# Kernel tuning notes

Measured on AMD Instinct MI355X. Metric: run time of the kernel, lower is better.

Reference implementation:

```python
import jax, jax.numpy as jnp
import numpy as np

EPS = 1e-5
NUM_CLASSES = 35
STYLE_LEN = 128


def conv3x3(x, w, b):
    # x: [B,C,H,W], w: [O,I,3,3] (OIHW), SAME padding, stride 1
    y = jax.lax.conv_general_dilated(x, w, (1, 1), 'SAME',
                                     dimension_numbers=('NCHW', 'OIHW', 'NCHW'))
    return y + b[None, :, None, None]


def instance_norm(x):
    # InstanceNorm2d(affine=False): per-sample, per-channel over H,W; biased var
    mu = jnp.mean(x, axis=(2, 3), keepdims=True)
    var = jnp.mean((x - mu) ** 2, axis=(2, 3), keepdims=True)
    return (x - mu) * jax.lax.rsqrt(var + EPS)


def setup_inputs() -> dict:
    key = jax.random.key(0)
    ks = jax.random.split(key, 20)
    B, C, H, W = 4, 256, 128, 256
    J, S = NUM_CLASSES, STYLE_LEN
    s = 0.05
    inp = {
        'x': jax.random.normal(ks[0], (B, C, H, W), jnp.float32),
        'seg_labels': jax.random.randint(ks[1], (B, H, W), 0, J),
        'style_codes': jax.random.normal(ks[2], (B, J, S), jnp.float32),
        # per-class FC: fc_w[j] is [out,in] like torch Linear
        'fc_w': jax.random.normal(ks[3], (J, S, S), jnp.float32) * s,
        'fc_b': jax.random.normal(ks[4], (J, S), jnp.float32) * s,
        'conv_gamma_w': jax.random.normal(ks[5], (C, S, 3, 3), jnp.float32) * s,
        'conv_gamma_b': jax.random.normal(ks[6], (C,), jnp.float32) * s,
        'conv_beta_w': jax.random.normal(ks[7], (C, S, 3, 3), jnp.float32) * s,
        'conv_beta_b': jax.random.normal(ks[8], (C,), jnp.float32) * s,
        # SPADE (sean=True): mlp_shared conv label_nc->128, then gamma/beta 128->C
        'mlp_w': jax.random.normal(ks[9], (128, J, 3, 3), jnp.float32) * s,
        'mlp_b': jax.random.normal(ks[10], (128,), jnp.float32) * s,
        'sp_gamma_w': jax.random.normal(ks[11], (C, 128, 3, 3), jnp.float32) * s,
        'sp_gamma_b': jax.random.normal(ks[12], (C,), jnp.float32) * s,
        'sp_beta_w': jax.random.normal(ks[13], (C, 128, 3, 3), jnp.float32) * s,
        'sp_beta_b': jax.random.normal(ks[14], (C,), jnp.float32) * s,
        'blending_gamma': jnp.zeros((1,), jnp.float32),
        'blending_beta': jnp.zeros((1,), jnp.float32),
    }
    return inp


def reference(x, seg_labels, style_codes, fc_w, fc_b,
              conv_gamma_w, conv_gamma_b, conv_beta_w, conv_beta_b,
              mlp_w, mlp_b, sp_gamma_w, sp_gamma_b, sp_beta_w, sp_beta_b,
              blending_gamma, blending_beta):
    # one-hot segmap [B,J,H,W]; same resolution as x so nearest interp is identity
    segmap = jax.nn.one_hot(seg_labels, NUM_CLASSES, axis=1, dtype=x.dtype)

    normalized = instance_norm(x)

    # per-class style FC: mu[b,j,:] = relu(fc_w[j] @ style_codes[b,j] + fc_b[j])
    mu = jax.nn.relu(jnp.einsum('bjd,jod->bjo', style_codes, fc_w) + fc_b[None])
    # gather-compute-scatter: each pixel receives the style vector of its class
    middle_avg = jnp.einsum('bjhw,bjc->bchw', segmap, mu)  # [B,128,H,W]

    gamma_avg = conv3x3(middle_avg, conv_gamma_w, conv_gamma_b)
    beta_avg = conv3x3(middle_avg, conv_beta_w, conv_beta_b)

    # SPADE branch (sean): gamma/beta from segmap
    actv = jax.nn.relu(conv3x3(segmap, mlp_w, mlp_b))
    gamma_spade = conv3x3(actv, sp_gamma_w, sp_gamma_b)
    beta_spade = conv3x3(actv, sp_beta_w, sp_beta_b)

    ga = jax.nn.sigmoid(blending_gamma)[0]
    ba = jax.nn.sigmoid(blending_beta)[0]
    gamma_final = ga * gamma_avg + (1 - ga) * gamma_spade
    beta_final = ba * beta_avg + (1 - ba) * beta_spade
    return normalized * (1 + gamma_final) + beta_final
```

## Files before the change

kernel.cpp:

```cpp
#include <hip/hip_runtime.h>
#include <stdint.h>

typedef __attribute__((ext_vector_type(8))) short short8;
typedef __attribute__((ext_vector_type(4))) float f32x4;

#define HP 130
#define WPAD 258
#define CIN 256

#define AS1 __attribute__((address_space(1)))
#define AS3 __attribute__((address_space(3)))

__device__ __forceinline__ unsigned short f2bf(float f) {
  unsigned int x = __float_as_uint(f);
  x = x + 0x7fffu + ((x >> 16) & 1u);
  return (unsigned short)(x >> 16);
}

__global__ __launch_bounds__(128) void k_mu(const float* __restrict__ sty,
    const float* __restrict__ fcw, const float* __restrict__ fcb,
    float* __restrict__ mu)
{
  int bj = blockIdx.x;
  int b = bj / 35, j = bj - 35 * b;
  int o = threadIdx.x;
  __shared__ float ss[128];
  ss[o] = sty[((size_t)b * 35 + j) * 128 + o];
  __syncthreads();
  const float4* wr = (const float4*)(fcw + ((size_t)j * 128 + o) * 128);
  const float4* sv = (const float4*)ss;
  float acc = fcb[j * 128 + o];
  #pragma unroll 8
  for (int d = 0; d < 32; ++d) {
    float4 wv = wr[d], s4 = sv[d];
    acc += wv.x * s4.x + wv.y * s4.y + wv.z * s4.z + wv.w * s4.w;
  }
  mu[((size_t)b * 35 + j) * 128 + o] = fmaxf(acc, 0.f);
}

__global__ __launch_bounds__(256) void k_prep(const float* __restrict__ mlpw,
    float* __restrict__ mlpT,
    const float* __restrict__ cgb, const float* __restrict__ cbb,
    const float* __restrict__ sgb, const float* __restrict__ sbb,
    const float* __restrict__ blg, const float* __restrict__ blb,
    float* __restrict__ bias)
{
  int t = blockIdx.x * 256 + threadIdx.x;
  if (t < 40320) {
    int o = t & 127;
    int jt = t >> 7;
    mlpT[(size_t)jt * 128 + o] = mlpw[((size_t)o * 35 + (jt / 9)) * 9 + (jt % 9)];
  }
  if (t < 256) {
    float ga = 1.f / (1.f + expf(-blg[0]));
    float ba = 1.f / (1.f + expf(-blb[0]));
    bias[t]       = ga * cgb[t] + (1.f - ga) * sgb[t];
    bias[256 + t] = ba * cbb[t] + (1.f - ba) * sbb[t];
  }
}

__global__ __launch_bounds__(256) void k_pack(
    const float* __restrict__ cgw, const float* __restrict__ cbw,
    const float* __restrict__ sgw, const float* __restrict__ sbw,
    const float* __restrict__ blg, const float* __restrict__ blb,
    unsigned short* __restrict__ Wp)
{
  int gid = blockIdx.x * 256 + threadIdx.x;
  int lane = gid & 63;
  int cc = (gid >> 6) & 7;
  int rest = gid >> 9;
  int tap = rest % 9;
  int vf = rest / 9;
  int v = vf * 16 + (lane & 15);
  int c = v >> 1, g = v & 1;
  int ci0 = cc * 32 + (lane >> 4) * 8;
  float ga = 1.f / (1.f + expf(-blg[0]));
  float ba = 1.f / (1.f + expf(-blb[0]));
  float sc = g ? ba : ga;
  const float* wavg = g ? cbw : cgw;
  const float* wsp  = g ? sbw : sgw;
  union { uint4 v4; unsigned short s[8]; } u;
  #pragma unroll
  for (int jj = 0; jj < 8; ++jj) {
    int ci = ci0 + jj;
    float val;
    if (ci < 128) val = sc * wavg[((size_t)c * 128 + ci) * 9 + tap];
    else          val = (1.f - sc) * wsp[((size_t)c * 128 + (ci - 128)) * 9 + tap];
    u.s[jj] = f2bf(val);
  }
  int vfgrp = vf >> 2, mfi = vf & 3;
  uint4* dst = (uint4*)Wp + ((size_t)(((vfgrp * 8 + cc) * 9 + tap) * 4 + mfi)) * 64 + lane;
  *dst = u.v4;
}

__global__ __launch_bounds__(256) void k_stats(const float* __restrict__ x,
                                               float* __restrict__ stats)
{
  int bc = blockIdx.x;
  const float* p = x + (size_t)bc * 32768;
  int t = threadIdx.x;
  float s = 0.f, s2 = 0.f;
  #pragma unroll 4
  for (int i = 0; i < 32; ++i) {
    float4 v = *(const float4*)(p + (size_t)i * 1024 + t * 4);
    s  += v.x + v.y + v.z + v.w;
    s2 += v.x * v.x + v.y * v.y + v.z * v.z + v.w * v.w;
  }
  #pragma unroll
  for (int off2 = 32; off2 > 0; off2 >>= 1) {
    s  += __shfl_down(s, off2);
    s2 += __shfl_down(s2, off2);
  }
  __shared__ float red[8];
  int lane = t & 63, wv = t >> 6;
  if (lane == 0) { red[wv] = s; red[4 + wv] = s2; }
  __syncthreads();
  if (t == 0) {
    float S  = red[0] + red[1] + red[2] + red[3];
    float S2 = red[4] + red[5] + red[6] + red[7];
    float mean = S * (1.f / 32768.f);
    float var  = S2 * (1.f / 32768.f) - mean * mean;
    stats[bc] = mean;
    stats[1024 + bc] = rsqrtf(var + 1e-5f);
  }
}

__global__ __launch_bounds__(256) void k_halo(uint4* __restrict__ U4)
{
  int t = blockIdx.x * 256 + threadIdx.x;
  if (t >= 98816) return;
  int sub = t & 31, pi = t >> 5;
  int b = pi / 772, r = pi - b * 772;
  int h, w;
  if (r < 258)      { h = 0;   w = r; }
  else if (r < 516) { h = 129; w = r - 258; }
  else if (r < 644) { h = r - 516 + 1; w = 0; }
  else              { h = r - 644 + 1; w = 257; }
  U4[((size_t)(b * HP + h) * WPAD + w) * 32 + sub] = (uint4){0, 0, 0, 0};
}

__global__ __launch_bounds__(256) void k_build(const int* __restrict__ seg,
    const float* __restrict__ mu, const float* __restrict__ mlpT,
    const float* __restrict__ mlpb, unsigned short* __restrict__ U)
{
  int blk = blockIdx.x;
  int b = blk >> 12, rem = blk & 4095;
  int h = rem >> 5, w0 = (rem & 31) << 3;
  int t = threadIdx.x;
  int p = t >> 5, q = t & 31;
  int w = w0 + p;
  unsigned short* up = U + (((size_t)(b * HP + h + 1)) * WPAD + (w + 1)) * CIN;
  union { uint4 v4; unsigned short s[8]; } u;
  if (q < 16) {
    int lab = seg[((size_t)b * 128 + h) * 256 + w];
    const float4* mrow = (const float4*)(mu + ((size_t)(b * 35 + lab)) * 128 + q * 8);
    float4 v0 = mrow[0], v1 = mrow[1];
    u.s[0] = f2bf(v0.x); u.s[1] = f2bf(v0.y); u.s[2] = f2bf(v0.z); u.s[3] = f2bf(v0.w);
    u.s[4] = f2bf(v1.x); u.s[5] = f2bf(v1.y); u.s[6] = f2bf(v1.z); u.s[7] = f2bf(v1.w);
    *(uint4*)(up + q * 8) = u.v4;
  } else {
    int o0 = (q - 16) * 8;
    float a[8];
    #pragma unroll
    for (int j = 0; j < 8; ++j) a[j] = mlpb[o0 + j];
    #pragma unroll
    for (int kh = 0; kh < 3; ++kh) {
      int hh = h + kh - 1;
      if ((unsigned)hh < 128u) {
        #pragma unroll
        for (int kw = 0; kw < 3; ++kw) {
          int ww = w + kw - 1;
          if ((unsigned)ww < 256u) {
            int lab2 = seg[((size_t)b * 128 + hh) * 256 + ww];
            const float4* wr = (const float4*)(mlpT + ((size_t)lab2 * 9 + kh * 3 + kw) * 128 + o0);
            float4 v0 = wr[0], v1 = wr[1];
            a[0] += v0.x; a[1] += v0.y; a[2] += v0.z; a[3] += v0.w;
            a[4] += v1.x; a[5] += v1.y; a[6] += v1.z; a[7] += v1.w;
          }
        }
      }
    }
    #pragma unroll
    for (int j = 0; j < 8; ++j) u.s[j] = f2bf(fmaxf(a[j], 0.f));
    *(uint4*)(up + 128 + o0) = u.v4;
  }
}


#define WAITV_(vm, lg) asm volatile("s_waitcnt vmcnt(" #vm ") lgkmcnt(" #lg ")" ::: "memory")
#define WAITV(vm, lg) do { WAITV_(vm, lg); __builtin_amdgcn_sched_barrier(0); } while (0)
#define WAITL(lg) do { asm volatile("s_waitcnt lgkmcnt(" #lg ")" ::: "memory"); __builtin_amdgcn_sched_barrier(0); } while (0)

#define MM(AS, BS, H) do {                                                     \
    __builtin_amdgcn_s_setprio(1);                                             \
    _Pragma("unroll")                                                          \
    for (int mf_ = 0; mf_ < 4; ++mf_)                                          \
      _Pragma("unroll")                                                        \
      for (int nf_ = 0; nf_ < 4; ++nf_)                                        \
        acc[mf_][(H) * 4 + nf_] = __builtin_amdgcn_mfma_f32_16x16x32_bf16(     \
            afr##AS[mf_], bfr##BS[nf_], acc[mf_][(H) * 4 + nf_], 0, 0, 0);     \
    __builtin_amdgcn_s_setprio(0);                                             \
  } while (0)

#define LOADA(NS) do {                                                         \
    aptr += 4096;                                                              \
    afr##NS[0] = *(const short8*)(aptr);                                       \
    afr##NS[1] = *(const short8*)(aptr + 1024);                                \
    afr##NS[2] = *(const short8*)(aptr + 2048);                                \
    afr##NS[3] = *(const short8*)(aptr + 3072);                                \
  } while (0)

#define LOADB(NS, T, H) do {                                                   \
    bfr##NS[0] = *(const short8*)(lbuf + off[T] + (H) * 4096);                 \
    bfr##NS[1] = *(const short8*)(lbuf + off[T] + (H) * 4096 + 1024);          \
    bfr##NS[2] = *(const short8*)(lbuf + off[T] + (H) * 4096 + 2048);          \
    bfr##NS[3] = *(const short8*)(lbuf + off[T] + (H) * 4096 + 3072);          \
  } while (0)

#define STG(SI) do {                                                           \
    __builtin_amdgcn_global_load_lds((const AS1 unsigned int*)gsrc[SI],        \
        (AS3 unsigned int*)((SI) < 6 ? (stbw + (SI) * 4096) : (stb + 24576)),  \
        16, 0, 0);                                                             \
    gsrc[SI] += 64;                                                            \
  } while (0)

__global__ __launch_bounds__(256, 2) void k_conv(
    const float* __restrict__ x, const uint4* __restrict__ U,
    const char* __restrict__ Wp, const float* __restrict__ bias,
    const float* __restrict__ stats, float* __restrict__ out)
{
  int bid = blockIdx.x;
  int xcd = bid & 7, i0 = bid >> 3;
  int pt = xcd * 128 + (i0 >> 1);
  int mt = i0 & 1;
  int b = pt >> 8, rem = pt & 255;
  int h0 = rem >> 1, w0 = (rem & 1) << 7;
  int tid = threadIdx.x;
  int lane = tid & 63, wid = tid >> 6;
  int lo = lane & 15, hi = lane >> 4;

  __shared__ uint4 Ubuf[2][1600];

  const char* gsrc[7];
  #pragma unroll
  for (int i = 0; i < 7; ++i) {
    int row = (i < 6) ? (wid + 4 * i) : 24;
    int slot = row * 64 + lane;
    int P = slot >> 2, sp = slot & 3;
    int sl = sp ^ ((P >> 1) & 3);
    int r = P / 130, pix = P - r * 130;
    gsrc[i] = (const char*)U +
        (size_t)(((b * HP + h0 + r) * WPAD + (w0 + pix)) * CIN + sl * 8) * 2;
  }

  f32x4 acc[4][8];
  #pragma unroll
  for (int i = 0; i < 4; ++i)
    #pragma unroll
    for (int j = 0; j < 8; ++j) acc[i][j] = (f32x4){0.f, 0.f, 0.f, 0.f};

  int vfgrp = mt * 4 + wid;
  const char* aptr = Wp + (size_t)vfgrp * 294912 + lane * 16;

  int off[9];
  #pragma unroll
  for (int t = 0; t < 9; ++t) {
    int Pb = (t / 3) * 130 + (t % 3) + lo;
    off[t] = Pb * 64 + ((hi ^ ((Pb >> 1) & 3)) << 4);
  }

  const char* lbuf = (const char*)&Ubuf[0][0];
  char* stb = (char*)&Ubuf[1][0];

  {
    char* stb0 = (char*)&Ubuf[0][0];
    char* stbw0 = stb0 + wid * 1024;
    #pragma unroll
    for (int i = 0; i < 7; ++i) {
      __builtin_amdgcn_global_load_lds((const AS1 unsigned int*)gsrc[i],
          (AS3 unsigned int*)(i < 6 ? (stbw0 + i * 4096) : (stb0 + 24576)), 16, 0, 0);
      gsrc[i] += 64;
    }
  }
  short8 afr0[4], afr1[4], bfr0[4], bfr1[4];
  afr0[0] = *(const short8*)(aptr);
  afr0[1] = *(const short8*)(aptr + 1024);
  afr0[2] = *(const short8*)(aptr + 2048);
  afr0[3] = *(const short8*)(aptr + 3072);
  WAITV(4, 0);
  __builtin_amdgcn_s_barrier();

  #pragma unroll 1
  for (int cc = 0; cc < 7; ++cc) {
    char* stbw = stb + wid * 1024;
    LOADB(0, 0, 0);
    LOADA(1); STG(0); LOADB(1, 0, 1); WAITV(5, 4); MM(0, 0, 0);
              LOADB(0, 1, 0);        WAITL(4);     MM(0, 1, 1);
    LOADA(0); STG(1); LOADB(1, 1, 1); WAITV(6, 4); MM(1, 0, 0);
              LOADB(0, 2, 0);        WAITL(4);     MM(1, 1, 1);
    LOADA(1); STG(2); LOADB(1, 2, 1); WAITV(6, 4); MM(0, 0, 0);
              LOADB(0, 3, 0);        WAITL(4);     MM(0, 1, 1);
    LOADA(0); STG(3); LOADB(1, 3, 1); WAITV(6, 4); MM(1, 0, 0);
              LOADB(0, 4, 0);        WAITL(4);     MM(1, 1, 1);
    LOADA(1); STG(4); LOADB(1, 4, 1); WAITV(6, 4); MM(0, 0, 0);
              LOADB(0, 5, 0);        WAITL(4);     MM(0, 1, 1);
    LOADA(0); STG(5); LOADB(1, 5, 1); WAITV(6, 4); MM(1, 0, 0);
              LOADB(0, 6, 0);        WAITL(4);     MM(1, 1, 1);
    LOADA(1); STG(6); LOADB(1, 6, 1); WAITV(6, 4); MM(0, 0, 0);
              LOADB(0, 7, 0);        WAITL(4);     MM(0, 1, 1);
    LOADA(0);         LOADB(1, 7, 1); WAITV(5, 4); MM(1, 0, 0);
              LOADB(0, 8, 0);        WAITL(4);     MM(1, 1, 1);
    LOADA(1);         LOADB(1, 8, 1); WAITV(4, 4); MM(0, 0, 0);
                                     WAITV(4, 0);  MM(0, 1, 1);
    __builtin_amdgcn_s_barrier();
    { const char* tmp = lbuf; lbuf = (const char*)stb; stb = (char*)tmp; }
    { short8 t0 = afr1[0]; afr0[0] = t0; t0 = afr1[1]; afr0[1] = t0;
      t0 = afr1[2]; afr0[2] = t0; t0 = afr1[3]; afr0[3] = t0; }
  }
  {
    LOADB(0, 0, 0);
    LOADA(1); LOADB(1, 0, 1); WAITV(4, 4); MM(0, 0, 0);
              LOADB(0, 1, 0); WAITL(4);    MM(0, 1, 1);
    LOADA(0); LOADB(1, 1, 1); WAITV(4, 4); MM(1, 0, 0);
              LOADB(0, 2, 0); WAITL(4);    MM(1, 1, 1);
    LOADA(1); LOADB(1, 2, 1); WAITV(4, 4); MM(0, 0, 0);
              LOADB(0, 3, 0); WAITL(4);    MM(0, 1, 1);
    LOADA(0); LOADB(1, 3, 1); WAITV(4, 4); MM(1, 0, 0);
              LOADB(0, 4, 0); WAITL(4);    MM(1, 1, 1);
    LOADA(1); LOADB(1, 4, 1); WAITV(4, 4); MM(0, 0, 0);
              LOADB(0, 5, 0); WAITL(4);    MM(0, 1, 1);
    LOADA(0); LOADB(1, 5, 1); WAITV(4, 4); MM(1, 0, 0);
              LOADB(0, 6, 0); WAITL(4);    MM(1, 1, 1);
    LOADA(1); LOADB(1, 6, 1); WAITV(4, 4); MM(0, 0, 0);
              LOADB(0, 7, 0); WAITL(4);    MM(0, 1, 1);
    LOADA(0); LOADB(1, 7, 1); WAITV(4, 4); MM(1, 0, 0);
              LOADB(0, 8, 0); WAITL(4);    MM(1, 1, 1);
              LOADB(1, 8, 1); WAITV(0, 4); MM(0, 0, 0);
                              WAITL(0);    MM(0, 1, 1);
  }

  #pragma unroll
  for (int mf = 0; mf < 4; ++mf) {
    int vbase = mt * 256 + wid * 64 + mf * 16 + hi * 4;
    #pragma unroll
    for (int p = 0; p < 2; ++p) {
      int c = (vbase >> 1) + p;
      float bg = bias[c], bb = bias[256 + c];
      float mean = stats[b * 256 + c], rs = stats[1024 + b * 256 + c];
      const float* xrow = x + ((size_t)(b * 256 + c) * 128 + h0) * 256 + w0;
      float* orow = out + ((size_t)(b * 256 + c) * 128 + h0) * 256 + w0;
      #pragma unroll
      for (int nf = 0; nf < 8; ++nf) {
        int pix = nf * 16 + lo;
        float g  = acc[mf][nf][2 * p]     + bg;
        float bt = acc[mf][nf][2 * p + 1] + bb;
        float xv = xrow[pix];
        orow[pix] = (xv - mean) * rs * (1.f + g) + bt;
      }
    }
  }
}

extern "C" void kernel_launch(void* const* d_in, const int* in_sizes, int n_in,
                              void* d_out, int out_size, void* d_ws, size_t ws_size,
                              hipStream_t stream)
{
  const float* x    = (const float*)d_in[0];
  const int*   seg  = (const int*)d_in[1];
  const float* sty  = (const float*)d_in[2];
  const float* fcw  = (const float*)d_in[3];
  const float* fcb  = (const float*)d_in[4];
  const float* cgw  = (const float*)d_in[5];
  const float* cgb  = (const float*)d_in[6];
  const float* cbw  = (const float*)d_in[7];
  const float* cbb  = (const float*)d_in[8];
  const float* mlpw = (const float*)d_in[9];
  const float* mlpb = (const float*)d_in[10];
  const float* sgw  = (const float*)d_in[11];
  const float* sgb  = (const float*)d_in[12];
  const float* sbw  = (const float*)d_in[13];
  const float* sbb  = (const float*)d_in[14];
  const float* blg  = (const float*)d_in[15];
  const float* blb  = (const float*)d_in[16];
  float* out = (float*)d_out;

  char* ws = (char*)d_ws;
  const size_t U_BYTES = (size_t)4 * HP * WPAD * CIN * 2;
  size_t off = 0;
  unsigned short* U = (unsigned short*)(ws + off); off += U_BYTES + 262144;
  char* Wp   = ws + off;           off += (size_t)512 * 256 * 9 * 2;
  float* mu  = (float*)(ws + off); off += (size_t)4 * 35 * 128 * 4;
  float* mlpT= (float*)(ws + off); off += (size_t)35 * 9 * 128 * 4;
  float* bias= (float*)(ws + off); off += 2048;
  float* stats=(float*)(ws + off); off += 8192;
  if (ws_size < off) return;

  k_halo <<<dim3(387),     dim3(256), 0, stream>>>((uint4*)U);
  k_mu   <<<dim3(140),     dim3(128), 0, stream>>>(sty, fcw, fcb, mu);
  k_prep <<<dim3(158),     dim3(256), 0, stream>>>(mlpw, mlpT, cgb, cbb, sgb, sbb, blg, blb, bias);
  k_pack <<<dim3(576),     dim3(256), 0, stream>>>(cgw, cbw, sgw, sbw, blg, blb, (unsigned short*)Wp);
  k_stats<<<dim3(1024),    dim3(256), 0, stream>>>(x, stats);
  k_build<<<dim3(16384),   dim3(256), 0, stream>>>(seg, mu, mlpT, mlpb, U);
  k_conv <<<dim3(2048),    dim3(256), 0, stream>>>(x, (const uint4*)U, Wp, bias, stats, out);
}
```

Before: 339.6 us.

## Switch conv GEMM from 16x16x32 to 32x32x16 MFMA with new LDS layout

```diff
diff --git a/kernel.cpp b/kernel.cpp
--- a/kernel.cpp
+++ b/kernel.cpp
@@ -2,7 +2,7 @@
 #include <stdint.h>
 
 typedef __attribute__((ext_vector_type(8))) short short8;
-typedef __attribute__((ext_vector_type(4))) float f32x4;
+typedef __attribute__((ext_vector_type(16))) float f32x16;
 
 #define HP 130
 #define WPAD 258
@@ -67,13 +67,16 @@
 {
   int gid = blockIdx.x * 256 + threadIdx.x;
   int lane = gid & 63;
-  int cc = (gid >> 6) & 7;
-  int rest = gid >> 9;
-  int tap = rest % 9;
-  int vf = rest / 9;
-  int v = vf * 16 + (lane & 15);
+  int sub = (gid >> 6) & 3;
+  int mf = sub >> 1, ks = sub & 1;
+  int u2 = gid >> 8;
+  int tap = u2 % 9;
+  int u3 = u2 / 9;
+  int cc = u3 & 7;
+  int vfgrp = u3 >> 3;
+  int v = vfgrp * 64 + mf * 32 + (lane & 31);
   int c = v >> 1, g = v & 1;
-  int ci0 = cc * 32 + (lane >> 4) * 8;
+  int ci0 = cc * 32 + ks * 16 + (lane >> 5) * 8;
   float ga = 1.f / (1.f + expf(-blg[0]));
   float ba = 1.f / (1.f + expf(-blb[0]));
   float sc = g ? ba : ga;
@@ -88,9 +91,7 @@
     else          val = (1.f - sc) * wsp[((size_t)c * 128 + (ci - 128)) * 9 + tap];
     u.s[jj] = f2bf(val);
   }
-  int vfgrp = vf >> 2, mfi = vf & 3;
-  uint4* dst = (uint4*)Wp + ((size_t)(((vfgrp * 8 + cc) * 9 + tap) * 4 + mfi)) * 64 + lane;
-  *dst = u.v4;
+  ((uint4*)Wp)[gid] = u.v4;
 }
 
 __global__ __launch_bounds__(256) void k_stats(const float* __restrict__ x,
@@ -191,14 +192,14 @@
 #define WAITV(vm, lg) do { WAITV_(vm, lg); __builtin_amdgcn_sched_barrier(0); } while (0)
 #define WAITL(lg) do { asm volatile("s_waitcnt lgkmcnt(" #lg ")" ::: "memory"); __builtin_amdgcn_sched_barrier(0); } while (0)
 
-#define MM(AS, BS, H) do {                                                     \
+#define MM(AS, BS, KS) do {                                                    \
     __builtin_amdgcn_s_setprio(1);                                             \
     _Pragma("unroll")                                                          \
-    for (int mf_ = 0; mf_ < 4; ++mf_)                                          \
+    for (int mf_ = 0; mf_ < 2; ++mf_)                                          \
       _Pragma("unroll")                                                        \
       for (int nf_ = 0; nf_ < 4; ++nf_)                                        \
-        acc[mf_][(H) * 4 + nf_] = __builtin_amdgcn_mfma_f32_16x16x32_bf16(     \
-            afr##AS[mf_], bfr##BS[nf_], acc[mf_][(H) * 4 + nf_], 0, 0, 0);     \
+        acc[mf_][nf_] = __builtin_amdgcn_mfma_f32_32x32x16_bf16(               \
+            afr##AS[mf_ * 2 + (KS)], bfr##BS[nf_], acc[mf_][nf_], 0, 0, 0);    \
     __builtin_amdgcn_s_setprio(0);                                             \
   } while (0)
 
@@ -210,11 +211,12 @@
     afr##NS[3] = *(const short8*)(aptr + 3072);                                \
   } while (0)
 
-#define LOADB(NS, T, H) do {                                                   \
-    bfr##NS[0] = *(const short8*)(lbuf + off[T] + (H) * 4096);                 \
-    bfr##NS[1] = *(const short8*)(lbuf + off[T] + (H) * 4096 + 1024);          \
-    bfr##NS[2] = *(const short8*)(lbuf + off[T] + (H) * 4096 + 2048);          \
-    bfr##NS[3] = *(const short8*)(lbuf + off[T] + (H) * 4096 + 3072);          \
+#define BOFF(T, KS) (((T) / 3) * 8320 + ((T) % 3) * 16 + (KS) * 4160)
+#define LOADB(NS, T, KS) do {                                                  \
+    bfr##NS[0] = *(const short8*)(lbuf + pbase + BOFF(T, KS));                 \
+    bfr##NS[1] = *(const short8*)(lbuf + pbase + BOFF(T, KS) + 512);           \
+    bfr##NS[2] = *(const short8*)(lbuf + pbase + BOFF(T, KS) + 1024);          \
+    bfr##NS[3] = *(const short8*)(lbuf + pbase + BOFF(T, KS) + 1536);          \
   } while (0)
 
 #define STG(SI) do {                                                           \
@@ -237,7 +239,7 @@
   int h0 = rem >> 1, w0 = (rem & 1) << 7;
   int tid = threadIdx.x;
   int lane = tid & 63, wid = tid >> 6;
-  int lo = lane & 15, hi = lane >> 4;
+  int lo32 = lane & 31, hi2 = lane >> 5;
 
   __shared__ uint4 Ubuf[2][1600];
 
@@ -245,29 +247,24 @@
   #pragma unroll
   for (int i = 0; i < 7; ++i) {
     int row = (i < 6) ? (wid + 4 * i) : 24;
-    int slot = row * 64 + lane;
-    int P = slot >> 2, sp = slot & 3;
-    int sl = sp ^ ((P >> 1) & 3);
-    int r = P / 130, pix = P - r * 130;
+    int L = row * 64 + lane;
+    int rsl = L / 130, px = L - rsl * 130;
+    int r = rsl >> 2, sl = rsl & 3;
     gsrc[i] = (const char*)U +
-        (size_t)(((b * HP + h0 + r) * WPAD + (w0 + pix)) * CIN + sl * 8) * 2;
-  }
-
-  f32x4 acc[4][8];
+        (size_t)(((b * HP + h0 + r) * WPAD + (w0 + px)) * CIN + sl * 8) * 2;
+  }
+
+  f32x16 acc[2][4];
+  const f32x16 vz = {0.f,0.f,0.f,0.f,0.f,0.f,0.f,0.f,0.f,0.f,0.f,0.f,0.f,0.f,0.f,0.f};
   #pragma unroll
-  for (int i = 0; i < 4; ++i)
-    #pragma unroll
-    for (int j = 0; j < 8; ++j) acc[i][j] = (f32x4){0.f, 0.f, 0.f, 0.f};
+  for (int i = 0; i < 2; ++i)
+    #pragma unroll
+    for (int j = 0; j < 4; ++j) acc[i][j] = vz;
 
   int vfgrp = mt * 4 + wid;
   const char* aptr = Wp + (size_t)vfgrp * 294912 + lane * 16;
 
-  int off[9];
-  #pragma unroll
-  for (int t = 0; t < 9; ++t) {
-    int Pb = (t / 3) * 130 + (t % 3) + lo;
-    off[t] = Pb * 64 + ((hi ^ ((Pb >> 1) & 3)) << 4);
-  }
+  int pbase = hi2 * 2080 + lo32 * 16;
 
   const char* lbuf = (const char*)&Ubuf[0][0];
   char* stb = (char*)&Ubuf[1][0];
@@ -340,20 +337,20 @@
   }
 
   #pragma unroll
-  for (int mf = 0; mf < 4; ++mf) {
-    int vbase = mt * 256 + wid * 64 + mf * 16 + hi * 4;
-    #pragma unroll
-    for (int p = 0; p < 2; ++p) {
-      int c = (vbase >> 1) + p;
+  for (int mf = 0; mf < 2; ++mf) {
+    int cbase = mt * 128 + wid * 32 + mf * 16;
+    #pragma unroll
+    for (int t = 0; t < 8; ++t) {
+      int c = cbase + (t & 1) + 4 * (t >> 1) + (hi2 << 1);
       float bg = bias[c], bb = bias[256 + c];
       float mean = stats[b * 256 + c], rs = stats[1024 + b * 256 + c];
       const float* xrow = x + ((size_t)(b * 256 + c) * 128 + h0) * 256 + w0;
       float* orow = out + ((size_t)(b * 256 + c) * 128 + h0) * 256 + w0;
       #pragma unroll
-      for (int nf = 0; nf < 8; ++nf) {
-        int pix = nf * 16 + lo;
-        float g  = acc[mf][nf][2 * p]     + bg;
-        float bt = acc[mf][nf][2 * p + 1] + bb;
+      for (int nf = 0; nf < 4; ++nf) {
+        int pix = nf * 32 + lo32;
+        float g  = acc[mf][nf][2 * t]     + bg;
+        float bt = acc[mf][nf][2 * t + 1] + bb;
         float xv = xrow[pix];
         orow[pix] = (xv - mean) * rs * (1.f + g) + bt;
       }
```

Result: slower. 383.9 us (+13.0%).
